# Kernel optimization log

Measured on AMD Instinct MI355X. Metric: run time of the kernel, lower is better.

Reference implementation:

```python
import jax, jax.numpy as jnp
import numpy as np

NOISE_STD = 0.1
TOP_K = 2


def setup_inputs() -> dict:
    key = jax.random.key(0)
    k_x, k_n, k_w, k_keys = jax.random.split(key, 4)
    N, D_IN, D_Q, K = 16384, 2048, 256, 64
    x = jax.random.normal(k_x, (N, D_IN), dtype=jnp.float32)
    noise = jax.random.normal(k_n, (N, K), dtype=jnp.float32)
    # Linear params (kaiming-uniform-ish scale) and xavier-uniform keys
    w_q = jax.random.normal(k_w, (D_IN, D_Q), dtype=jnp.float32) * (1.0 / np.sqrt(D_IN))
    b_q = jnp.zeros((D_Q,), dtype=jnp.float32)
    lim = np.sqrt(6.0 / (K + D_Q))
    keys = jax.random.uniform(k_keys, (K, D_Q), dtype=jnp.float32, minval=-lim, maxval=lim)
    return {"x": x, "noise": noise, "w_q": w_q, "b_q": b_q, "keys": keys}


def reference(x, noise, w_q, b_q, keys):
    # query projection: [N, D_in] @ [D_in, D_q] -> [N, D_q]
    query = x @ w_q + b_q
    d_q = query.shape[-1]
    # router logits: [N, K], scaled dot product with expert keys
    logits = (query @ keys.T) * (1.0 / jnp.sqrt(jnp.asarray(d_q, query.dtype)))
    logits = logits + noise * NOISE_STD  # training-mode gating noise
    # top-k selection + softmax over selected logits only
    top_logits, top_idx = jax.lax.top_k(logits, TOP_K)       # [N, top_k]
    top_probs = jax.nn.softmax(top_logits, axis=-1)           # [N, top_k]
    # scatter selected probs into dense [N, K] gating tensor (zeros elsewhere)
    rows = jnp.arange(logits.shape[0])[:, None]               # [N, 1]
    gating_probs = jnp.zeros_like(logits).at[rows, top_idx].set(top_probs)
    return gating_probs, top_idx
```

## Files before the change

### kernel.cpp

```cpp
#include <hip/hip_runtime.h>

#define MROWS 16384
#define KD 2048
#define NQ 256
#define NE 64
#define INV_SQRT_DQ 0.0625f
#define NOISE_STD_C 0.1f

typedef _Float16 f16x8 __attribute__((ext_vector_type(8)));
typedef float f32x4 __attribute__((ext_vector_type(4)));

__device__ inline void split8(const float4& a, const float4& b, f16x8* h, f16x8* l) {
    float v[8] = {a.x, a.y, a.z, a.w, b.x, b.y, b.z, b.w};
    f16x8 hh, ll;
#pragma unroll
    for (int i = 0; i < 8; ++i) {
        _Float16 s = (_Float16)v[i];
        hh[i] = s;
        ll[i] = (_Float16)(v[i] - (float)s);
    }
    *h = hh;
    *l = ll;
}

__global__ void prep_w(const float* __restrict__ w, _Float16* __restrict__ whp,
                       _Float16* __restrict__ wlp) {
    const int tid = blockIdx.x * 256 + threadIdx.x;
    const int f    = tid & 15;
    const int q    = (tid >> 4) & 3;
    const int ngrp = (tid >> 6) & 15;
    const int kcs  = tid >> 10;
    const int n = ngrp * 16 + f;
    const int k = kcs * 32 + q * 8;
    f16x8 h, l;
#pragma unroll
    for (int j = 0; j < 8; ++j) {
        float v = w[(size_t)(k + j) * NQ + n];
        _Float16 s = (_Float16)v;
        h[j] = s;
        l[j] = (_Float16)(v - (float)s);
    }
    *(f16x8*)(whp + (size_t)tid * 8) = h;
    *(f16x8*)(wlp + (size_t)tid * 8) = l;
}

__global__ __launch_bounds__(512) void gemm_fused(
    const float* __restrict__ x, const _Float16* __restrict__ whp,
    const _Float16* __restrict__ wlp, const float* __restrict__ bq,
    const float* __restrict__ keys, const float* __restrict__ noise,
    float* __restrict__ gate, float* __restrict__ idxout) {
    __shared__ __align__(16) char smem[85248];
    _Float16* Ah = (_Float16*)smem;
    _Float16* Al = (_Float16*)(smem + 8192);
    float* LG = (float*)smem;
    float* qs = (float*)(smem + 16640);

    const int t = threadIdx.x;
    const int lane = t & 63;
    const int wv = t >> 6;
    const int m0 = blockIdx.x * 64;
    const int f = lane & 15;
    const int qq = lane >> 4;

    const int srow = t >> 3;
    const int sk8 = (t & 7) * 8;
    const int scol = sk8 ^ ((srow & 7) * 8);
    const float* xp = x + (size_t)(m0 + srow) * KD + sk8;

    f32x4 acc[4][2];
#pragma unroll
    for (int mt = 0; mt < 4; ++mt)
#pragma unroll
        for (int nt = 0; nt < 2; ++nt) acc[mt][nt] = {0.f, 0.f, 0.f, 0.f};

    float4 pfA = *(const float4*)xp;
    float4 pfB = *(const float4*)(xp + 4);

    const int aswz = (f & 7) * 8;

    for (int i = 0; i < 32; ++i) {
        __syncthreads();
        f16x8 h8, l8;
        split8(pfA, pfB, &h8, &l8);
        *(f16x8*)(Ah + srow * 64 + scol) = h8;
        *(f16x8*)(Al + srow * 64 + scol) = l8;
        __syncthreads();
        if (i < 31) {
            pfA = *(const float4*)(xp + (i + 1) * 64);
            pfB = *(const float4*)(xp + (i + 1) * 64 + 4);
        }
        f16x8 bh[2][2], bl[2][2];
#pragma unroll
        for (int ks = 0; ks < 2; ++ks)
#pragma unroll
            for (int nt = 0; nt < 2; ++nt) {
                size_t o = ((size_t)((2 * i + ks) * 16 + 2 * wv + nt) * 64 + lane) * 8;
                bh[ks][nt] = *(const f16x8*)(whp + o);
                bl[ks][nt] = *(const f16x8*)(wlp + o);
            }
#pragma unroll
        for (int ks = 0; ks < 2; ++ks) {
            f16x8 ah[4], al[4];
#pragma unroll
            for (int mt = 0; mt < 4; ++mt) {
                int ab = (mt * 16 + f) * 64 + ((ks * 32 + qq * 8) ^ aswz);
                ah[mt] = *(const f16x8*)(Ah + ab);
                al[mt] = *(const f16x8*)(Al + ab);
            }
#pragma unroll
            for (int mt = 0; mt < 4; ++mt)
#pragma unroll
                for (int nt = 0; nt < 2; ++nt) {
                    acc[mt][nt] = __builtin_amdgcn_mfma_f32_16x16x32_f16(ah[mt], bh[ks][nt], acc[mt][nt], 0, 0, 0);
                    acc[mt][nt] = __builtin_amdgcn_mfma_f32_16x16x32_f16(ah[mt], bl[ks][nt], acc[mt][nt], 0, 0, 0);
                    acc[mt][nt] = __builtin_amdgcn_mfma_f32_16x16x32_f16(al[mt], bh[ks][nt], acc[mt][nt], 0, 0, 0);
                }
        }
    }

#pragma unroll
    for (int nt = 0; nt < 2; ++nt) {
        int col = wv * 32 + nt * 16 + f;
        float bias = bq[col];
#pragma unroll
        for (int mt = 0; mt < 4; ++mt)
#pragma unroll
            for (int r = 0; r < 4; ++r)
                qs[(mt * 16 + qq * 4 + r) * 268 + col] = acc[mt][nt][r] + bias;
    }
    __syncthreads();

    if (wv < 4) {
        f32x4 a2[4];
#pragma unroll
        for (int mt = 0; mt < 4; ++mt) a2[mt] = {0.f, 0.f, 0.f, 0.f};
        const int e = wv * 16 + f;
        const float* kp = keys + (size_t)e * NQ + qq * 8;
        for (int kc = 0; kc < NQ; kc += 32) {
            float4 b0 = *(const float4*)(kp + kc);
            float4 b1 = *(const float4*)(kp + kc + 4);
            f16x8 bh2, bl2;
            split8(b0, b1, &bh2, &bl2);
#pragma unroll
            for (int mt = 0; mt < 4; ++mt) {
                const float* ap = qs + (mt * 16 + f) * 268 + kc + qq * 8;
                float4 a0 = *(const float4*)ap;
                float4 a1 = *(const float4*)(ap + 4);
                f16x8 ah2, al2;
                split8(a0, a1, &ah2, &al2);
                a2[mt] = __builtin_amdgcn_mfma_f32_16x16x32_f16(ah2, bh2, a2[mt], 0, 0, 0);
                a2[mt] = __builtin_amdgcn_mfma_f32_16x16x32_f16(ah2, bl2, a2[mt], 0, 0, 0);
                a2[mt] = __builtin_amdgcn_mfma_f32_16x16x32_f16(al2, bh2, a2[mt], 0, 0, 0);
            }
        }
#pragma unroll
        for (int mt = 0; mt < 4; ++mt)
#pragma unroll
            for (int r = 0; r < 4; ++r) {
                int row = mt * 16 + qq * 4 + r;
                LG[row * 65 + e] = a2[mt][r] * INV_SQRT_DQ +
                                   NOISE_STD_C * noise[(size_t)(m0 + row) * NE + e];
            }
    }
    __syncthreads();

    for (int i = 0; i < 8; ++i) {
        int r = wv * 8 + i;
        float v = LG[r * 65 + lane];
        float v1 = v; int i1 = lane;
#pragma unroll
        for (int off = 32; off; off >>= 1) {
            float ov = __shfl_xor(v1, off);
            int oi = __shfl_xor(i1, off);
            if (ov > v1 || (ov == v1 && oi < i1)) { v1 = ov; i1 = oi; }
        }
        float v2 = (lane == i1) ? -1e30f : v;
        int i2 = lane;
#pragma unroll
        for (int off = 32; off; off >>= 1) {
            float ov = __shfl_xor(v2, off);
            int oi = __shfl_xor(i2, off);
            if (ov > v2 || (ov == v2 && oi < i2)) { v2 = ov; i2 = oi; }
        }
        float ex = expf(v2 - v1);
        float p1 = 1.0f / (1.0f + ex);
        float p2 = ex * p1;
        float g = (lane == i1) ? p1 : ((lane == i2) ? p2 : 0.0f);
        gate[(size_t)(m0 + r) * NE + lane] = g;
        if (lane == 0) {
            float2 ii = make_float2((float)i1, (float)i2);
            *(float2*)(idxout + (size_t)(m0 + r) * 2) = ii;
        }
    }
}

extern "C" void kernel_launch(void* const* d_in, const int* in_sizes, int n_in,
                              void* d_out, int out_size, void* d_ws, size_t ws_size,
                              hipStream_t stream) {
    const float* x     = (const float*)d_in[0];
    const float* noise = (const float*)d_in[1];
    const float* w_q   = (const float*)d_in[2];
    const float* b_q   = (const float*)d_in[3];
    const float* keys  = (const float*)d_in[4];
    float* out = (float*)d_out;

    char* ws = (char*)d_ws;
    _Float16* whp = (_Float16*)ws;
    _Float16* wlp = (_Float16*)(ws + (1u << 20));

    prep_w<<<256, 256, 0, stream>>>(w_q, whp, wlp);
    gemm_fused<<<256, 512, 0, stream>>>(x, whp, wlp, b_q, keys, noise,
                                        out, out + (size_t)MROWS * NE);
}
```

Measured before the change: 259.0 us.

## Double-buffer A tile in LDS and register-prefetch W fragments

The main GEMM loop now double-buffers the split fp16 A tile in shared memory, with one barrier per iteration instead of two. The next iteration's W fragments are prefetched into registers and x is loaded two steps ahead with nontemporal loads. LDS is shrunk by aliasing the query buffer at offset 0, which needs an extra barrier before the logits write, and the qs stride drops from 268 to 260. The aim is to hide global-load latency behind MFMA work, at the cost of more registers and a possible occupancy drop.

```diff
diff --git a/kernel.cpp b/kernel.cpp
--- a/kernel.cpp
+++ b/kernel.cpp
@@ -10,17 +10,19 @@
 typedef _Float16 f16x8 __attribute__((ext_vector_type(8)));
 typedef float f32x4 __attribute__((ext_vector_type(4)));
 
-__device__ inline void split8(const float4& a, const float4& b, f16x8* h, f16x8* l) {
-    float v[8] = {a.x, a.y, a.z, a.w, b.x, b.y, b.z, b.w};
+__device__ inline void split8v(f32x4 a, f32x4 b, f16x8* h, f16x8* l) {
     f16x8 hh, ll;
 #pragma unroll
-    for (int i = 0; i < 8; ++i) {
-        _Float16 s = (_Float16)v[i];
-        hh[i] = s;
-        ll[i] = (_Float16)(v[i] - (float)s);
-    }
-    *h = hh;
-    *l = ll;
+    for (int i = 0; i < 4; ++i) {
+        _Float16 s = (_Float16)a[i];
+        hh[i] = s; ll[i] = (_Float16)(a[i] - (float)s);
+    }
+#pragma unroll
+    for (int i = 0; i < 4; ++i) {
+        _Float16 s = (_Float16)b[i];
+        hh[4 + i] = s; ll[4 + i] = (_Float16)(b[i] - (float)s);
+    }
+    *h = hh; *l = ll;
 }
 
 __global__ void prep_w(const float* __restrict__ w, _Float16* __restrict__ whp,
@@ -49,11 +51,7 @@
     const _Float16* __restrict__ wlp, const float* __restrict__ bq,
     const float* __restrict__ keys, const float* __restrict__ noise,
     float* __restrict__ gate, float* __restrict__ idxout) {
-    __shared__ __align__(16) char smem[85248];
-    _Float16* Ah = (_Float16*)smem;
-    _Float16* Al = (_Float16*)(smem + 8192);
-    float* LG = (float*)smem;
-    float* qs = (float*)(smem + 16640);
+    __shared__ __align__(16) char smem[66560];
 
     const int t = threadIdx.x;
     const int lane = t & 63;
@@ -61,11 +59,15 @@
     const int m0 = blockIdx.x * 64;
     const int f = lane & 15;
     const int qq = lane >> 4;
+    const int aswz = (f & 7) * 8;
 
     const int srow = t >> 3;
     const int sk8 = (t & 7) * 8;
     const int scol = sk8 ^ ((srow & 7) * 8);
-    const float* xp = x + (size_t)(m0 + srow) * KD + sk8;
+    const f32x4* xp = (const f32x4*)(x + (size_t)(m0 + srow) * KD + sk8);
+
+    const _Float16* bph = whp + (size_t)(2 * wv) * 512 + lane * 8;
+    const _Float16* bpl = wlp + (size_t)(2 * wv) * 512 + lane * 8;
 
     f32x4 acc[4][2];
 #pragma unroll
@@ -73,51 +75,88 @@
 #pragma unroll
         for (int nt = 0; nt < 2; ++nt) acc[mt][nt] = {0.f, 0.f, 0.f, 0.f};
 
-    float4 pfA = *(const float4*)xp;
-    float4 pfB = *(const float4*)(xp + 4);
-
-    const int aswz = (f & 7) * 8;
+    f16x8 bhC[2][2], blC[2][2], bhN[2][2], blN[2][2];
+
+    f32x4 xa = __builtin_nontemporal_load(xp);
+    f32x4 xb = __builtin_nontemporal_load(xp + 1);
+#pragma unroll
+    for (int ks = 0; ks < 2; ++ks)
+#pragma unroll
+        for (int nt = 0; nt < 2; ++nt) {
+            size_t o = (size_t)ks * 8192 + nt * 512;
+            bhC[ks][nt] = *(const f16x8*)(bph + o);
+            blC[ks][nt] = *(const f16x8*)(bpl + o);
+        }
+    {
+        f16x8 h8, l8;
+        split8v(xa, xb, &h8, &l8);
+        *(f16x8*)((_Float16*)smem + srow * 64 + scol) = h8;
+        *(f16x8*)((_Float16*)(smem + 8192) + srow * 64 + scol) = l8;
+    }
+    xa = __builtin_nontemporal_load(xp + 16);
+    xb = __builtin_nontemporal_load(xp + 17);
+    __syncthreads();
 
     for (int i = 0; i < 32; ++i) {
-        __syncthreads();
-        f16x8 h8, l8;
-        split8(pfA, pfB, &h8, &l8);
-        *(f16x8*)(Ah + srow * 64 + scol) = h8;
-        *(f16x8*)(Al + srow * 64 + scol) = l8;
-        __syncthreads();
-        if (i < 31) {
-            pfA = *(const float4*)(xp + (i + 1) * 64);
-            pfB = *(const float4*)(xp + (i + 1) * 64 + 4);
-        }
-        f16x8 bh[2][2], bl[2][2];
-#pragma unroll
-        for (int ks = 0; ks < 2; ++ks)
-#pragma unroll
-            for (int nt = 0; nt < 2; ++nt) {
-                size_t o = ((size_t)((2 * i + ks) * 16 + 2 * wv + nt) * 64 + lane) * 8;
-                bh[ks][nt] = *(const f16x8*)(whp + o);
-                bl[ks][nt] = *(const f16x8*)(wlp + o);
-            }
+        const int cb = i & 1;
+        _Float16* AhC = (_Float16*)(smem + cb * 16384);
+        _Float16* AlC = AhC + 4096;
+        _Float16* AhN = (_Float16*)(smem + (cb ^ 1) * 16384);
+        _Float16* AlN = AhN + 4096;
+
+        if (i + 1 < 32) {
+            size_t base = (size_t)(2 * (i + 1)) * 8192;
+#pragma unroll
+            for (int ks = 0; ks < 2; ++ks)
+#pragma unroll
+                for (int nt = 0; nt < 2; ++nt) {
+                    size_t o = base + (size_t)ks * 8192 + nt * 512;
+                    bhN[ks][nt] = *(const f16x8*)(bph + o);
+                    blN[ks][nt] = *(const f16x8*)(bpl + o);
+                }
+        }
+        if (i + 1 < 32) {
+            f16x8 h8, l8;
+            split8v(xa, xb, &h8, &l8);
+            *(f16x8*)(AhN + srow * 64 + scol) = h8;
+            *(f16x8*)(AlN + srow * 64 + scol) = l8;
+        }
+        if (i + 2 < 32) {
+            xa = __builtin_nontemporal_load(xp + (i + 2) * 16);
+            xb = __builtin_nontemporal_load(xp + (i + 2) * 16 + 1);
+        }
 #pragma unroll
         for (int ks = 0; ks < 2; ++ks) {
             f16x8 ah[4], al[4];
 #pragma unroll
             for (int mt = 0; mt < 4; ++mt) {
                 int ab = (mt * 16 + f) * 64 + ((ks * 32 + qq * 8) ^ aswz);
-                ah[mt] = *(const f16x8*)(Ah + ab);
-                al[mt] = *(const f16x8*)(Al + ab);
+                ah[mt] = *(const f16x8*)(AhC + ab);
+                al[mt] = *(const f16x8*)(AlC + ab);
             }
 #pragma unroll
             for (int mt = 0; mt < 4; ++mt)
 #pragma unroll
                 for (int nt = 0; nt < 2; ++nt) {
-                    acc[mt][nt] = __builtin_amdgcn_mfma_f32_16x16x32_f16(ah[mt], bh[ks][nt], acc[mt][nt], 0, 0, 0);
-                    acc[mt][nt] = __builtin_amdgcn_mfma_f32_16x16x32_f16(ah[mt], bl[ks][nt], acc[mt][nt], 0, 0, 0);
-                    acc[mt][nt] = __builtin_amdgcn_mfma_f32_16x16x32_f16(al[mt], bh[ks][nt], acc[mt][nt], 0, 0, 0);
+                    acc[mt][nt] = __builtin_amdgcn_mfma_f32_16x16x32_f16(ah[mt], bhC[ks][nt], acc[mt][nt], 0, 0, 0);
+                    acc[mt][nt] = __builtin_amdgcn_mfma_f32_16x16x32_f16(ah[mt], blC[ks][nt], acc[mt][nt], 0, 0, 0);
+                    acc[mt][nt] = __builtin_amdgcn_mfma_f32_16x16x32_f16(al[mt], bhC[ks][nt], acc[mt][nt], 0, 0, 0);
                 }
         }
-    }
-
+#pragma unroll
+        for (int ks = 0; ks < 2; ++ks)
+#pragma unroll
+            for (int nt = 0; nt < 2; ++nt) {
+                bhC[ks][nt] = bhN[ks][nt];
+                blC[ks][nt] = blN[ks][nt];
+            }
+        asm volatile("" ::: "memory");
+        __builtin_amdgcn_s_waitcnt(0xC07F);
+        __builtin_amdgcn_s_barrier();
+        asm volatile("" ::: "memory");
+    }
+
+    float* qs = (float*)smem;
 #pragma unroll
     for (int nt = 0; nt < 2; ++nt) {
         int col = wv * 32 + nt * 16 + f;
@@ -126,33 +165,38 @@
         for (int mt = 0; mt < 4; ++mt)
 #pragma unroll
             for (int r = 0; r < 4; ++r)
-                qs[(mt * 16 + qq * 4 + r) * 268 + col] = acc[mt][nt][r] + bias;
-    }
-    __syncthreads();
-
+                qs[(mt * 16 + qq * 4 + r) * 260 + col] = acc[mt][nt][r] + bias;
+    }
+    __syncthreads();
+
+    const int e = wv * 16 + f;
+    f32x4 a2[4];
+#pragma unroll
+    for (int mt = 0; mt < 4; ++mt) a2[mt] = {0.f, 0.f, 0.f, 0.f};
     if (wv < 4) {
-        f32x4 a2[4];
-#pragma unroll
-        for (int mt = 0; mt < 4; ++mt) a2[mt] = {0.f, 0.f, 0.f, 0.f};
-        const int e = wv * 16 + f;
         const float* kp = keys + (size_t)e * NQ + qq * 8;
         for (int kc = 0; kc < NQ; kc += 32) {
-            float4 b0 = *(const float4*)(kp + kc);
-            float4 b1 = *(const float4*)(kp + kc + 4);
+            f32x4 b0 = *(const f32x4*)(kp + kc);
+            f32x4 b1 = *(const f32x4*)(kp + kc + 4);
             f16x8 bh2, bl2;
-            split8(b0, b1, &bh2, &bl2);
+            split8v(b0, b1, &bh2, &bl2);
 #pragma unroll
             for (int mt = 0; mt < 4; ++mt) {
-                const float* ap = qs + (mt * 16 + f) * 268 + kc + qq * 8;
-                float4 a0 = *(const float4*)ap;
-                float4 a1 = *(const float4*)(ap + 4);
+                const float* ap = qs + (mt * 16 + f) * 260 + kc + qq * 8;
+                f32x4 a0 = *(const f32x4*)ap;
+                f32x4 a1 = *(const f32x4*)(ap + 4);
                 f16x8 ah2, al2;
-                split8(a0, a1, &ah2, &al2);
+                split8v(a0, a1, &ah2, &al2);
                 a2[mt] = __builtin_amdgcn_mfma_f32_16x16x32_f16(ah2, bh2, a2[mt], 0, 0, 0);
                 a2[mt] = __builtin_amdgcn_mfma_f32_16x16x32_f16(ah2, bl2, a2[mt], 0, 0, 0);
                 a2[mt] = __builtin_amdgcn_mfma_f32_16x16x32_f16(al2, bh2, a2[mt], 0, 0, 0);
             }
         }
+    }
+    __syncthreads();
+
+    float* LG = (float*)smem;
+    if (wv < 4) {
 #pragma unroll
         for (int mt = 0; mt < 4; ++mt)
 #pragma unroll
```

After: 231.6 us. 1.12x faster.
